# Kernel tuning notes

Measured on AMD Instinct MI355X. Metric: run time of the kernel, lower is better.

## Reference

```python
import jax, jax.numpy as jnp
import numpy as np

NODE_DIM = 8
IN_EDGE_DIM = 4
OUT_EDGE_DIM = 4
HID = 16
N_NODES = 100000
N_EDGES = 3200000
LN_EPS = 1e-5


def _layer_norm(h, gamma, beta):
    mu = jnp.mean(h, axis=-1, keepdims=True)
    var = jnp.mean(jnp.square(h - mu), axis=-1, keepdims=True)
    return (h - mu) * jax.lax.rsqrt(var + LN_EPS) * gamma + beta


def setup_inputs() -> dict:
    key = jax.random.key(0)
    ks = jax.random.split(key, 12)
    in_dim = NODE_DIM * 2 + IN_EDGE_DIM  # 20
    x = jax.random.normal(ks[0], (N_NODES, NODE_DIM), dtype=jnp.float32)
    edge_index = jax.random.randint(ks[1], (2, N_EDGES), 0, N_NODES, dtype=jnp.int64)
    edge_attr = jax.random.normal(ks[2], (N_EDGES, IN_EDGE_DIM), dtype=jnp.float32)
    # MLP params (Kaiming-uniform-ish scaling like torch defaults)
    def lin(k, fan_in, fan_out):
        lim = 1.0 / np.sqrt(fan_in)
        kw, kb = jax.random.split(k)
        W = jax.random.uniform(kw, (fan_in, fan_out), minval=-lim, maxval=lim, dtype=jnp.float32)
        b = jax.random.uniform(kb, (fan_out,), minval=-lim, maxval=lim, dtype=jnp.float32)
        return W, b
    W1, b1 = lin(ks[3], in_dim, HID)
    W2, b2 = lin(ks[4], HID, HID)
    W3, b3 = lin(ks[5], HID, OUT_EDGE_DIM)
    g1 = jnp.ones((HID,), jnp.float32); be1 = jnp.zeros((HID,), jnp.float32)
    g2 = jnp.ones((HID,), jnp.float32); be2 = jnp.zeros((HID,), jnp.float32)
    return {"x": x, "edge_index": edge_index, "edge_attr": edge_attr,
            "W1": W1, "b1": b1, "g1": g1, "be1": be1,
            "W2": W2, "b2": b2, "g2": g2, "be2": be2,
            "W3": W3, "b3": b3}


def reference(x, edge_index, edge_attr, W1, b1, g1, be1, W2, b2, g2, be2, W3, b3):
    frm = edge_index[0]
    to = edge_index[1]
    # gather node features for both endpoints, concat with edge features: [E, 2*node_dim+in_edge_dim]
    inpt = jnp.concatenate([x[frm], x[to], edge_attr.astype(jnp.float32)], axis=1)
    h = _layer_norm(jax.nn.relu(inpt @ W1 + b1), g1, be1)
    h = _layer_norm(jax.nn.relu(h @ W2 + b2), g2, be2)
    return h @ W3 + b3  # [E, out_edge_dim]
```

## Files before the change

### kernel.cpp

```cpp
#include <hip/hip_runtime.h>
#include <stdint.h>


using u16 = unsigned short;
using u32 = uint32_t;
typedef __attribute__((ext_vector_type(4))) float f32x4;
typedef __attribute__((ext_vector_type(8))) short bf16x8;
typedef __attribute__((ext_vector_type(2))) __bf16 bf16x2;

__device__ __forceinline__ float bf2f(u16 u) { return __uint_as_float(((u32)u) << 16); }
__device__ __forceinline__ float bflo(u32 u) { return __uint_as_float(u << 16); }
__device__ __forceinline__ float bfhi(u32 u) { return __uint_as_float(u & 0xFFFF0000u); }
__device__ __forceinline__ u32 f2bf(float f) {
    u32 u = __float_as_uint(f);
    return (u + 0x7FFFu + ((u >> 16) & 1u)) >> 16;
}
__device__ __forceinline__ u32 pkbf(float a, float b) {
    bf16x2 t;
    t.x = (__bf16)a;
    t.y = (__bf16)b;
    return __builtin_bit_cast(u32, t);
}
__device__ __forceinline__ float ldw(const void* p, int i, bool bf) {
    return bf ? bf2f(((const u16*)p)[i]) : ((const float*)p)[i];
}

#define WB_W1 0
#define WB_B1 320
#define WB_W2 336
#define WB_B2 592
#define WB_W3 608
#define WB_B3 672
#define WB_TOT 704
#define WB_ZRG 676
#define FQ_A1H 0
#define FQ_A1L 512
#define FQ_A2X 1024
#define FQ_A2Y 1536
#define FQ_A3X 2048
#define FQ_A3Y 2560
#define FB_OFF (WB_TOT + 1536)

__global__ __launch_bounds__(256)
void probe_convert(const int* __restrict__ ei, int n_pairs,
                   const void* W1, const void* b1, const void* g1, const void* be1,
                   const void* W2, const void* b2, const void* g2, const void* be2,
                   const void* W3, const void* b3,
                   int* __restrict__ flags, float* __restrict__ wb) {
    bool bf = (((const u32*)g1)[0] == 0x3F803F80u);
    __shared__ int s;
    if (threadIdx.x == 0) s = 0;
    __syncthreads();
    int limit = n_pairs < 2048 ? n_pairs : 2048;
    int found = 0;
    for (int i = threadIdx.x; i < limit; i += blockDim.x)
        if (ei[2 * i + 1] != 0) found = 1;
    if (found) s = 1;
    __syncthreads();
    if (threadIdx.x == 0) { flags[0] = s; flags[1] = bf ? 1 : 0; }

    int t = threadIdx.x;
    for (int i = t; i < 320; i += 256) wb[WB_W1 + i] = ldw(W1, i, bf);
    if (t < 16) wb[WB_B1 + t] = ldw(b1, t, bf);
    {
        int k = t >> 4;
        wb[WB_W2 + t] = ldw(g1, k, bf) * ldw(W2, t, bf);
    }
    if (t < 16) {
        float acc = ldw(b2, t, bf);
        for (int k = 0; k < 16; k++) acc = fmaf(ldw(be1, k, bf), ldw(W2, k * 16 + t, bf), acc);
        wb[WB_B2 + t] = acc;
    }
    if (t < 64) {
        int k = t >> 2;
        wb[WB_W3 + t] = ldw(g2, k, bf) * ldw(W3, t, bf);
    }
    if (t < 4) {
        float acc = ldw(b3, t, bf);
        for (int k = 0; k < 16; k++) acc = fmaf(ldw(be2, k, bf), ldw(W3, k * 4 + t, bf), acc);
        wb[WB_B3 + t] = acc;
    }
    if (t >= 4 && t < 32) wb[672 + t] = 0.f;

    __syncthreads();

    u16* fq = (u16*)(wb + WB_TOT);
    for (int i = t; i < 512; i += 256) {
        int l = i >> 3, j = i & 7;
        int m = l & 15, g = l >> 4;
        int k1 = g * 8 + j;
        float w1 = (k1 < 20) ? wb[WB_W1 + k1 * 16 + m] : 0.f;
        u16 h1 = (u16)f2bf(w1);
        fq[FQ_A1H + i] = h1;
        fq[FQ_A1L + i] = (u16)f2bf(w1 - bf2f(h1));

        int k2 = g * 4 + (j & 3);
        int part = j >> 2;
        float w2 = wb[WB_W2 + k2 * 16 + m];
        u16 h2 = (u16)f2bf(w2);
        u16 l2v = (u16)f2bf(w2 - bf2f(h2));
        fq[FQ_A2X + i] = part ? l2v : h2;
        fq[FQ_A2Y + i] = part ? h2 : l2v;

        float w3 = (m < 4) ? wb[WB_W3 + k2 * 4 + m] : 0.f;
        u16 h3 = (u16)f2bf(w3);
        u16 l3v = (u16)f2bf(w3 - bf2f(h3));
        fq[FQ_A3X + i] = part ? l3v : h3;
        fq[FQ_A3Y + i] = part ? h3 : l3v;
    }
    {
        float* fbv = wb + FB_OFF;
        int l = t >> 2, r = t & 3;
        int row = ((l >> 4) << 2) + r;
        fbv[t] = wb[WB_B1 + row];
        fbv[256 + t] = wb[WB_B2 + row];
        fbv[512 + t] = (row < 4) ? wb[WB_B3 + row] : 0.f;
    }
}

__device__ __forceinline__ void ln16(f32x4 d, float& h0, float& h1, float& h2, float& h3) {
    f32x4 z = {0.f, 0.f, 0.f, 0.f};
    d = __builtin_elementwise_max(d, z);
    float s = (d.x + d.y) + (d.z + d.w);
    float q = fmaf(d.x, d.x, fmaf(d.y, d.y, fmaf(d.z, d.z, d.w * d.w)));
    s += __shfl_xor(s, 16);
    q += __shfl_xor(q, 16);
    s += __shfl_xor(s, 32);
    q += __shfl_xor(q, 32);
    float mu = s * 0.0625f;
    float var = fmaf(-mu, mu, q * 0.0625f);
    float r = rsqrtf(var + 1e-5f);
    float nb = -mu * r;
    h0 = fmaf(d.x, r, nb);
    h1 = fmaf(d.y, r, nb);
    h2 = fmaf(d.z, r, nb);
    h3 = fmaf(d.w, r, nb);
}

__device__ __forceinline__ bf16x8 packB(float h0, float h1, float h2, float h3) {
    u32 hi01 = pkbf(h0, h1), hi23 = pkbf(h2, h3);
    u32 lo01 = pkbf(h0 - bflo(hi01), h1 - bfhi(hi01));
    u32 lo23 = pkbf(h2 - bflo(hi23), h3 - bfhi(hi23));
    return __builtin_bit_cast(bf16x8, make_uint4(hi01, hi23, lo01, lo23));
}

#define TPW 8

__global__ __launch_bounds__(256, 4)
void edge_mlp_mfma(const void* __restrict__ x, const int* __restrict__ ei,
                   const void* __restrict__ ea, const float* __restrict__ wb,
                   const int* __restrict__ flags, void* __restrict__ out, int n_edges) {
    const bool idx32 = flags[0] != 0;
    const bool bf = flags[1] != 0;

    const int lane = threadIdx.x & 63;
    const int n = lane & 15;
    const int g = lane >> 4;

    const u16* fq = (const u16*)(wb + WB_TOT);
    bf16x8 A1h = ((const bf16x8*)fq)[0 * 64 + lane];
    bf16x8 A1l = ((const bf16x8*)fq)[1 * 64 + lane];
    bf16x8 A2x = ((const bf16x8*)fq)[2 * 64 + lane];
    bf16x8 A2y = ((const bf16x8*)fq)[3 * 64 + lane];
    bf16x8 A3x = ((const bf16x8*)fq)[4 * 64 + lane];
    bf16x8 A3y = ((const bf16x8*)fq)[5 * 64 + lane];
    const f32x4* fb = (const f32x4*)(wb + FB_OFF);
    f32x4 pb1 = fb[lane];
    f32x4 pb2 = fb[64 + lane];
    f32x4 pb3 = fb[128 + lane];

    const char* zrg = (const char*)(wb + WB_ZRG);
    const size_t eoff = (g == 1) ? (size_t)n_edges : 0;

    const int ntiles = (n_edges + 15) >> 4;
    const int wflat = blockIdx.x * 4 + (threadIdx.x >> 6);
    const int t0 = wflat * TPW;

#pragma unroll 2
    for (int ti = 0; ti < TPW; ++ti) {
        int tile = t0 + ti;
        if (tile >= ntiles) break;

        int e = (tile << 4) + n;
        bool ev = e < n_edges;
        int ec = ev ? e : (n_edges - 1);

        int idx = 0;
        if (g < 2) {
            size_t col = eoff + (size_t)ec;
            idx = idx32 ? ei[col] : ei[2 * col];
        }

        f32x4 d1 = pb1;
        if (bf) {
            const uint4* pA = (g < 2)
                ? (const uint4*)((const char*)x + (size_t)idx * 16)
                : (const uint4*)zrg;
            const uint2* pE = (g == 2)
                ? (const uint2*)((const char*)ea + (size_t)ec * 8)
                : (const uint2*)zrg;
            uint4 r16 = *pA;
            uint2 r8 = *pE;
            uint4 braw = make_uint4(r16.x | r8.x, r16.y | r8.y, r16.z, r16.w);
            d1 = __builtin_amdgcn_mfma_f32_16x16x32_bf16(
                A1h, __builtin_bit_cast(bf16x8, braw), d1, 0, 0, 0);
        } else {
            const float4* pA = (g < 2)
                ? (const float4*)((const char*)x + (size_t)idx * 32)
                : ((g == 2) ? (const float4*)((const char*)ea + (size_t)ec * 16)
                            : (const float4*)zrg);
            const float4* pB = (g < 2) ? (pA + 1) : (const float4*)zrg;
            float4 a = *pA;
            float4 b = *pB;
            u32 h01 = pkbf(a.x, a.y), h23 = pkbf(a.z, a.w);
            u32 h45 = pkbf(b.x, b.y), h67 = pkbf(b.z, b.w);
            u32 l01 = pkbf(a.x - bflo(h01), a.y - bfhi(h01));
            u32 l23 = pkbf(a.z - bflo(h23), a.w - bfhi(h23));
            u32 l45 = pkbf(b.x - bflo(h45), b.y - bfhi(h45));
            u32 l67 = pkbf(b.z - bflo(h67), b.w - bfhi(h67));
            bf16x8 Bh = __builtin_bit_cast(bf16x8, make_uint4(h01, h23, h45, h67));
            bf16x8 Bl = __builtin_bit_cast(bf16x8, make_uint4(l01, l23, l45, l67));
            d1 = __builtin_amdgcn_mfma_f32_16x16x32_bf16(A1h, Bh, d1, 0, 0, 0);
            d1 = __builtin_amdgcn_mfma_f32_16x16x32_bf16(A1h, Bl, d1, 0, 0, 0);
            d1 = __builtin_amdgcn_mfma_f32_16x16x32_bf16(A1l, Bh, d1, 0, 0, 0);
        }

        float h0, h1, h2, h3;
        ln16(d1, h0, h1, h2, h3);

        bf16x8 B2 = packB(h0, h1, h2, h3);
        f32x4 d2 = pb2;
        d2 = __builtin_amdgcn_mfma_f32_16x16x32_bf16(A2x, B2, d2, 0, 0, 0);
        d2 = __builtin_amdgcn_mfma_f32_16x16x32_bf16(A2y, B2, d2, 0, 0, 0);
        float z0, z1, z2, z3;
        ln16(d2, z0, z1, z2, z3);

        bf16x8 B3 = packB(z0, z1, z2, z3);
        f32x4 d3 = pb3;
        d3 = __builtin_amdgcn_mfma_f32_16x16x32_bf16(A3x, B3, d3, 0, 0, 0);
        d3 = __builtin_amdgcn_mfma_f32_16x16x32_bf16(A3y, B3, d3, 0, 0, 0);

        if (g == 0 && ev) {
            if (bf) {
                u32 p0 = pkbf(d3.x, d3.y);
                u32 p1 = pkbf(d3.z, d3.w);
                ((uint2*)out)[e] = make_uint2(p0, p1);
            } else {
                ((float4*)out)[e] = make_float4(d3.x, d3.y, d3.z, d3.w);
            }
        }
    }
}

extern "C" void kernel_launch(void* const* d_in, const int* in_sizes, int n_in,
                              void* d_out, int out_size, void* d_ws, size_t ws_size,
                              hipStream_t stream) {
    const void* x  = d_in[0];
    const int* ei  = (const int*)d_in[1];
    const void* ea = d_in[2];

    int n_edges = in_sizes[1] / 2;

    int* flags = (int*)d_ws;
    float* wb = (float*)((char*)d_ws + 64);

    probe_convert<<<1, 256, 0, stream>>>(ei, n_edges,
                                         d_in[3], d_in[4], d_in[5], d_in[6],
                                         d_in[7], d_in[8], d_in[9], d_in[10],
                                         d_in[11], d_in[12], flags, wb);

    int ntiles = (n_edges + 15) / 16;
    int mblocks = (ntiles + 4 * TPW - 1) / (4 * TPW);
    edge_mlp_mfma<<<mblocks, 256, 0, stream>>>(x, ei, ea, wb, flags, d_out, n_edges);
}
```

Baseline: 227.1 us.

## Batch gathers for two tiles before compute and raise occupancy target

```diff
diff --git a/kernel.cpp b/kernel.cpp
--- a/kernel.cpp
+++ b/kernel.cpp
@@ -146,7 +146,7 @@
 
 #define TPW 8
 
-__global__ __launch_bounds__(256, 4)
+__global__ __launch_bounds__(256, 6)
 void edge_mlp_mfma(const void* __restrict__ x, const int* __restrict__ ei,
                    const void* __restrict__ ea, const float* __restrict__ wb,
                    const int* __restrict__ flags, void* __restrict__ out, int n_edges) {
@@ -175,78 +175,111 @@
     const int ntiles = (n_edges + 15) >> 4;
     const int wflat = blockIdx.x * 4 + (threadIdx.x >> 6);
     const int t0 = wflat * TPW;
-
-#pragma unroll 2
-    for (int ti = 0; ti < TPW; ++ti) {
-        int tile = t0 + ti;
-        if (tile >= ntiles) break;
-
-        int e = (tile << 4) + n;
-        bool ev = e < n_edges;
-        int ec = ev ? e : (n_edges - 1);
-
-        int idx = 0;
+    if (t0 >= ntiles) return;
+
+#pragma unroll 1
+    for (int ti = 0; ti < TPW; ti += 2) {
+        asm volatile("" : "+v"(A1h), "+v"(A1l), "+v"(A2x), "+v"(A2y), "+v"(A3x),
+                          "+v"(A3y), "+v"(pb1), "+v"(pb2), "+v"(pb3));
+
+        int tileA = t0 + ti;
+        int tileB = tileA + 1;
+        if (tileA >= ntiles) break;
+        bool haveB = tileB < ntiles;
+
+        int eA = (tileA << 4) + n;
+        int eB = (tileB << 4) + n;
+        bool evA = eA < n_edges;
+        bool evB = haveB && (eB < n_edges);
+        int ecA = evA ? eA : (n_edges - 1);
+        int ecB = evB ? eB : (n_edges - 1);
+
+        int idxA = 0, idxB = 0;
         if (g < 2) {
-            size_t col = eoff + (size_t)ec;
-            idx = idx32 ? ei[col] : ei[2 * col];
+            idxA = idx32 ? ei[eoff + (size_t)ecA] : ei[2 * (eoff + (size_t)ecA)];
+            idxB = idx32 ? ei[eoff + (size_t)ecB] : ei[2 * (eoff + (size_t)ecB)];
         }
 
-        f32x4 d1 = pb1;
+        float4 aA, bA, aB, bB;
+        uint4 rA16, rB16;
+        uint2 rA8, rB8;
         if (bf) {
-            const uint4* pA = (g < 2)
-                ? (const uint4*)((const char*)x + (size_t)idx * 16)
-                : (const uint4*)zrg;
-            const uint2* pE = (g == 2)
-                ? (const uint2*)((const char*)ea + (size_t)ec * 8)
-                : (const uint2*)zrg;
-            uint4 r16 = *pA;
-            uint2 r8 = *pE;
-            uint4 braw = make_uint4(r16.x | r8.x, r16.y | r8.y, r16.z, r16.w);
-            d1 = __builtin_amdgcn_mfma_f32_16x16x32_bf16(
-                A1h, __builtin_bit_cast(bf16x8, braw), d1, 0, 0, 0);
+            const uint4* pA = (g < 2) ? (const uint4*)((const char*)x + (size_t)idxA * 16)
+                                      : (const uint4*)zrg;
+            const uint2* pEA = (g == 2) ? (const uint2*)((const char*)ea + (size_t)ecA * 8)
+                                        : (const uint2*)zrg;
+            const uint4* pB = (g < 2) ? (const uint4*)((const char*)x + (size_t)idxB * 16)
+                                      : (const uint4*)zrg;
+            const uint2* pEB = (g == 2) ? (const uint2*)((const char*)ea + (size_t)ecB * 8)
+                                        : (const uint2*)zrg;
+            rA16 = *pA; rA8 = *pEA;
+            rB16 = *pB; rB8 = *pEB;
         } else {
-            const float4* pA = (g < 2)
-                ? (const float4*)((const char*)x + (size_t)idx * 32)
-                : ((g == 2) ? (const float4*)((const char*)ea + (size_t)ec * 16)
-                            : (const float4*)zrg);
-            const float4* pB = (g < 2) ? (pA + 1) : (const float4*)zrg;
-            float4 a = *pA;
-            float4 b = *pB;
-            u32 h01 = pkbf(a.x, a.y), h23 = pkbf(a.z, a.w);
-            u32 h45 = pkbf(b.x, b.y), h67 = pkbf(b.z, b.w);
-            u32 l01 = pkbf(a.x - bflo(h01), a.y - bfhi(h01));
-            u32 l23 = pkbf(a.z - bflo(h23), a.w - bfhi(h23));
-            u32 l45 = pkbf(b.x - bflo(h45), b.y - bfhi(h45));
-            u32 l67 = pkbf(b.z - bflo(h67), b.w - bfhi(h67));
-            bf16x8 Bh = __builtin_bit_cast(bf16x8, make_uint4(h01, h23, h45, h67));
-            bf16x8 Bl = __builtin_bit_cast(bf16x8, make_uint4(l01, l23, l45, l67));
-            d1 = __builtin_amdgcn_mfma_f32_16x16x32_bf16(A1h, Bh, d1, 0, 0, 0);
-            d1 = __builtin_amdgcn_mfma_f32_16x16x32_bf16(A1h, Bl, d1, 0, 0, 0);
-            d1 = __builtin_amdgcn_mfma_f32_16x16x32_bf16(A1l, Bh, d1, 0, 0, 0);
+            const float4* pA = (g < 2) ? (const float4*)((const char*)x + (size_t)idxA * 32)
+                             : ((g == 2) ? (const float4*)((const char*)ea + (size_t)ecA * 16)
+                                         : (const float4*)zrg);
+            const float4* pA2 = (g < 2) ? (pA + 1) : (const float4*)zrg;
+            const float4* pB = (g < 2) ? (const float4*)((const char*)x + (size_t)idxB * 32)
+                             : ((g == 2) ? (const float4*)((const char*)ea + (size_t)ecB * 16)
+                                         : (const float4*)zrg);
+            const float4* pB2 = (g < 2) ? (pB + 1) : (const float4*)zrg;
+            aA = *pA; bA = *pA2;
+            aB = *pB; bB = *pB2;
         }
 
-        float h0, h1, h2, h3;
-        ln16(d1, h0, h1, h2, h3);
-
-        bf16x8 B2 = packB(h0, h1, h2, h3);
-        f32x4 d2 = pb2;
-        d2 = __builtin_amdgcn_mfma_f32_16x16x32_bf16(A2x, B2, d2, 0, 0, 0);
-        d2 = __builtin_amdgcn_mfma_f32_16x16x32_bf16(A2y, B2, d2, 0, 0, 0);
-        float z0, z1, z2, z3;
-        ln16(d2, z0, z1, z2, z3);
-
-        bf16x8 B3 = packB(z0, z1, z2, z3);
-        f32x4 d3 = pb3;
-        d3 = __builtin_amdgcn_mfma_f32_16x16x32_bf16(A3x, B3, d3, 0, 0, 0);
-        d3 = __builtin_amdgcn_mfma_f32_16x16x32_bf16(A3y, B3, d3, 0, 0, 0);
-
-        if (g == 0 && ev) {
+#pragma unroll
+        for (int half = 0; half < 2; ++half) {
+            bool live = (half == 0) ? true : haveB;
+            if (!live) break;
+            bool ev = (half == 0) ? evA : evB;
+            int e = (half == 0) ? eA : eB;
+
+            f32x4 d1 = pb1;
             if (bf) {
-                u32 p0 = pkbf(d3.x, d3.y);
-                u32 p1 = pkbf(d3.z, d3.w);
-                ((uint2*)out)[e] = make_uint2(p0, p1);
+                uint4 r16 = (half == 0) ? rA16 : rB16;
+                uint2 r8 = (half == 0) ? rA8 : rB8;
+                uint4 braw = make_uint4(r16.x | r8.x, r16.y | r8.y, r16.z, r16.w);
+                d1 = __builtin_amdgcn_mfma_f32_16x16x32_bf16(
+                    A1h, __builtin_bit_cast(bf16x8, braw), d1, 0, 0, 0);
             } else {
-                ((float4*)out)[e] = make_float4(d3.x, d3.y, d3.z, d3.w);
+                float4 a = (half == 0) ? aA : aB;
+                float4 b = (half == 0) ? bA : bB;
+                u32 h01 = pkbf(a.x, a.y), h23 = pkbf(a.z, a.w);
+                u32 h45 = pkbf(b.x, b.y), h67 = pkbf(b.z, b.w);
+                u32 l01 = pkbf(a.x - bflo(h01), a.y - bfhi(h01));
+                u32 l23 = pkbf(a.z - bflo(h23), a.w - bfhi(h23));
+                u32 l45 = pkbf(b.x - bflo(h45), b.y - bfhi(h45));
+                u32 l67 = pkbf(b.z - bflo(h67), b.w - bfhi(h67));
+                bf16x8 Bh = __builtin_bit_cast(bf16x8, make_uint4(h01, h23, h45, h67));
+                bf16x8 Bl = __builtin_bit_cast(bf16x8, make_uint4(l01, l23, l45, l67));
+                d1 = __builtin_amdgcn_mfma_f32_16x16x32_bf16(A1h, Bh, d1, 0, 0, 0);
+                d1 = __builtin_amdgcn_mfma_f32_16x16x32_bf16(A1h, Bl, d1, 0, 0, 0);
+                d1 = __builtin_amdgcn_mfma_f32_16x16x32_bf16(A1l, Bh, d1, 0, 0, 0);
+            }
+
+            float h0, h1, h2, h3;
+            ln16(d1, h0, h1, h2, h3);
+
+            bf16x8 B2 = packB(h0, h1, h2, h3);
+            f32x4 d2 = pb2;
+            d2 = __builtin_amdgcn_mfma_f32_16x16x32_bf16(A2x, B2, d2, 0, 0, 0);
+            d2 = __builtin_amdgcn_mfma_f32_16x16x32_bf16(A2y, B2, d2, 0, 0, 0);
+            float z0, z1, z2, z3;
+            ln16(d2, z0, z1, z2, z3);
+
+            bf16x8 B3 = packB(z0, z1, z2, z3);
+            f32x4 d3 = pb3;
+            d3 = __builtin_amdgcn_mfma_f32_16x16x32_bf16(A3x, B3, d3, 0, 0, 0);
+            d3 = __builtin_amdgcn_mfma_f32_16x16x32_bf16(A3y, B3, d3, 0, 0, 0);
+
+            if (g == 0 && ev) {
+                if (bf) {
+                    u32 p0 = pkbf(d3.x, d3.y);
+                    u32 p1 = pkbf(d3.z, d3.w);
+                    ((uint2*)out)[e] = make_uint2(p0, p1);
+                } else {
+                    ((float4*)out)[e] = make_float4(d3.x, d3.y, d3.z, d3.w);
+                }
             }
         }
     }
```

Result: slower. 379.9 us (+67.2%).
